# Performance work log

Measured on AMD Instinct MI355X. Metric: run time of the kernel, lower is better.

## Reference

```python
import jax, jax.numpy as jnp
import numpy as np


def setup_inputs() -> dict:
    key = jax.random.key(0)
    ks = jax.random.split(key, 5)
    b, f, h, w, c = 2, 16, 64, 64, 256
    heads, D = 8, 32
    hD = heads * D
    x = jax.random.normal(ks[0], (b, f, h, w, c), dtype=jnp.float32)
    s = 1.0 / np.sqrt(c)
    Wq = jax.random.normal(ks[1], (c, hD), dtype=jnp.float32) * s
    Wk = jax.random.normal(ks[2], (c, hD), dtype=jnp.float32) * s
    Wv = jax.random.normal(ks[3], (c, hD), dtype=jnp.float32) * s
    Wo = jax.random.normal(ks[4], (hD, c), dtype=jnp.float32) * s
    return {"x": x, "Wq": Wq, "Wk": Wk, "Wv": Wv, "Wo": Wo, "heads": heads}


def reference(x, Wq, Wk, Wv, Wo, heads):
    b, f, h, w, c = x.shape
    hD = Wq.shape[1]
    D = hD // heads
    n = h * w
    # fuse batch & frames; 1x1 conv == channel matmul
    xf = x.reshape(b * f, n, c)  # [(bf), n, c]

    def proj(W):
        # [(bf), n, hD] -> [(bf), heads, D, n]
        p = jnp.einsum('bnc,cd->bnd', xf, W)
        return p.reshape(b * f, n, heads, D).transpose(0, 2, 3, 1)

    q = jax.nn.softmax(proj(Wq), axis=-2)  # softmax over D (note: scale is dead code in source)
    k = jax.nn.softmax(proj(Wk), axis=-1)  # softmax over spatial n
    v = proj(Wv)
    context = jnp.einsum('bhdn,bhen->bhde', k, v)      # [(bf), heads, D, D]
    out = jnp.einsum('bhde,bhdn->bhen', context, q)    # [(bf), heads, D, n]
    out = out.transpose(0, 3, 1, 2).reshape(b * f, n, hD)
    out = jnp.einsum('bnd,dc->bnc', out, Wo)
    return out.reshape(b, f, h, w, c)
```

## Files before the change

kernel.cpp:

```cpp
#include <hip/hip_runtime.h>
#include <hip/hip_bf16.h>


typedef __attribute__((ext_vector_type(8))) short bf16x8;
typedef __attribute__((ext_vector_type(4))) float f32x4;

__device__ __forceinline__ unsigned short f2bf(float x) {
  __hip_bfloat16 h = __float2bfloat16(x);
  union { __hip_bfloat16 b; unsigned short u; } c; c.b = h; return c.u;
}

__global__ __launch_bounds__(256) void k0_prep(const float* __restrict__ Wq,
                                               const float* __restrict__ Wk,
                                               const float* __restrict__ Wv,
                                               unsigned short* __restrict__ WqT,
                                               unsigned short* __restrict__ WkvT) {
  int r = blockIdx.x, c = threadIdx.x;
  if (r < 256)      WqT [(r      )*256 + c] = f2bf(Wq[c*256 + r]);
  else if (r < 512) WkvT[(r - 256)*256 + c] = f2bf(Wk[c*256 + (r-256)]);
  else              WkvT[(r - 256)*256 + c] = f2bf(Wv[c*256 + (r-512)]);
}

__global__ __launch_bounds__(512, 2) void k1p(const float* __restrict__ x,
                                              const unsigned short* __restrict__ WkvT,
                                              float* __restrict__ ctxp) {
  __shared__ unsigned short As[2][32*256];
  __shared__ unsigned short slab[2][512*32];
  int bid = blockIdx.x;
  size_t rowbase = (size_t)bid * 256;
  int tid = threadIdx.x;
  int lane = tid & 63, wid = tid >> 6;
  int cl = lane & 15, rq = (lane >> 4) << 2, fs = lane >> 4;

  bf16x8 bfr[4][8];
#pragma unroll
  for (int nf = 0; nf < 4; ++nf)
#pragma unroll
    for (int kk = 0; kk < 8; ++kk)
      bfr[nf][kk] = *(const bf16x8*)(WkvT + (size_t)(wid*64 + nf*16 + cl)*256 + kk*32 + fs*8);

  f32x4 c2a = {}, c2b = {}, c2c = {}, c2d = {};
  f32x4 c3a = {}, c3b = {};
  bf16x8 bone;
#pragma unroll
  for (int j = 0; j < 8; ++j) bone[j] = (short)0x3F80;

  int ar = tid >> 5, as_ = tid & 31;
  int aw0 = ar*256 + ((as_ ^ (ar & 7)) << 3);
  int aw1 = (16 + ar)*256 + ((as_ ^ (ar & 7)) << 3);
  const float* ap = x + (rowbase + ar)*256 + as_*8;

  int ca0 = wid*32 + cl,        ca1 = wid*32 + 16 + cl;
  int cb0 = 256 + wid*32 + cl,  cb1 = 256 + wid*32 + 16 + cl;
  int ra0 = ca0*32 + ((fs ^ ((ca0 ^ (ca0 >> 2)) & 3)) << 3);
  int ra1 = ca1*32 + ((fs ^ ((ca1 ^ (ca1 >> 2)) & 3)) << 3);
  int rb0 = cb0*32 + ((fs ^ ((cb0 ^ (cb0 >> 2)) & 3)) << 3);
  int rb1 = cb1*32 + ((fs ^ ((cb1 ^ (cb1 >> 2)) & 3)) << 3);

  f32x4 acc0[4], acc1[4];

  float4 pa0 = *(const float4*)ap;
  float4 pa1 = *(const float4*)(ap + 4);
  float4 pa2 = *(const float4*)(ap + 16*256);
  float4 pa3 = *(const float4*)(ap + 16*256 + 4);
  {
    unsigned short* Ab = &As[0][0];
    union { ushort4 u4[2]; int4 i4; } pk;
    pk.u4[0].x = f2bf(pa0.x); pk.u4[0].y = f2bf(pa0.y); pk.u4[0].z = f2bf(pa0.z); pk.u4[0].w = f2bf(pa0.w);
    pk.u4[1].x = f2bf(pa1.x); pk.u4[1].y = f2bf(pa1.y); pk.u4[1].z = f2bf(pa1.z); pk.u4[1].w = f2bf(pa1.w);
    *(int4*)(&Ab[aw0]) = pk.i4;
    pk.u4[0].x = f2bf(pa2.x); pk.u4[0].y = f2bf(pa2.y); pk.u4[0].z = f2bf(pa2.z); pk.u4[0].w = f2bf(pa2.w);
    pk.u4[1].x = f2bf(pa3.x); pk.u4[1].y = f2bf(pa3.y); pk.u4[1].z = f2bf(pa3.z); pk.u4[1].w = f2bf(pa3.w);
    *(int4*)(&Ab[aw1]) = pk.i4;
  }
  {
    const float* apn = ap + 32*256;
    pa0 = *(const float4*)apn;
    pa1 = *(const float4*)(apn + 4);
    pa2 = *(const float4*)(apn + 16*256);
    pa3 = *(const float4*)(apn + 16*256 + 4);
  }
  __syncthreads();
  {
    unsigned short* Ab = &As[0][0];
#pragma unroll
    for (int ni = 0; ni < 4; ++ni) { acc0[ni] = (f32x4){}; acc1[ni] = (f32x4){}; }
#pragma unroll
    for (int kk = 0; kk < 8; ++kk) {
      int so = (((kk*4 + fs) ^ (cl & 7)) << 3);
      bf16x8 a0 = *(const bf16x8*)(&Ab[cl*256 + so]);
      bf16x8 a1 = *(const bf16x8*)(&Ab[(16 + cl)*256 + so]);
#pragma unroll
      for (int ni = 0; ni < 4; ++ni) {
        acc0[ni] = __builtin_amdgcn_mfma_f32_16x16x32_bf16(a0, bfr[ni][kk], acc0[ni], 0, 0, 0);
        acc1[ni] = __builtin_amdgcn_mfma_f32_16x16x32_bf16(a1, bfr[ni][kk], acc1[ni], 0, 0, 0);
      }
    }
  }

  for (int t = 0; t < 7; ++t) {
    {
      unsigned short* sb = &slab[t & 1][0];
#pragma unroll
      for (int ni = 0; ni < 4; ++ni) {
        int c = wid*64 + ni*16 + cl;
        int sw = (c ^ (c >> 2)) & 3;
        ushort4 w0, w1;
        if (wid < 4) {
          w0.x = f2bf(__expf(acc0[ni][0])); w0.y = f2bf(__expf(acc0[ni][1]));
          w0.z = f2bf(__expf(acc0[ni][2])); w0.w = f2bf(__expf(acc0[ni][3]));
          w1.x = f2bf(__expf(acc1[ni][0])); w1.y = f2bf(__expf(acc1[ni][1]));
          w1.z = f2bf(__expf(acc1[ni][2])); w1.w = f2bf(__expf(acc1[ni][3]));
        } else {
          w0.x = f2bf(acc0[ni][0]); w0.y = f2bf(acc0[ni][1]);
          w0.z = f2bf(acc0[ni][2]); w0.w = f2bf(acc0[ni][3]);
          w1.x = f2bf(acc1[ni][0]); w1.y = f2bf(acc1[ni][1]);
          w1.z = f2bf(acc1[ni][2]); w1.w = f2bf(acc1[ni][3]);
        }
        *(ushort4*)(&sb[c*32 + (((rq >> 3) ^ sw) << 3) + (rq & 7)]) = w0;
        *(ushort4*)(&sb[c*32 + ((((16 + rq) >> 3) ^ sw) << 3) + (rq & 7)]) = w1;
      }
    }
    {
      unsigned short* Ab = &As[(t + 1) & 1][0];
      union { ushort4 u4[2]; int4 i4; } pk;
      pk.u4[0].x = f2bf(pa0.x); pk.u4[0].y = f2bf(pa0.y); pk.u4[0].z = f2bf(pa0.z); pk.u4[0].w = f2bf(pa0.w);
      pk.u4[1].x = f2bf(pa1.x); pk.u4[1].y = f2bf(pa1.y); pk.u4[1].z = f2bf(pa1.z); pk.u4[1].w = f2bf(pa1.w);
      *(int4*)(&Ab[aw0]) = pk.i4;
      pk.u4[0].x = f2bf(pa2.x); pk.u4[0].y = f2bf(pa2.y); pk.u4[0].z = f2bf(pa2.z); pk.u4[0].w = f2bf(pa2.w);
      pk.u4[1].x = f2bf(pa3.x); pk.u4[1].y = f2bf(pa3.y); pk.u4[1].z = f2bf(pa3.z); pk.u4[1].w = f2bf(pa3.w);
      *(int4*)(&Ab[aw1]) = pk.i4;
    }
    if (t < 6) {
      const float* apn = ap + (size_t)(t + 2)*32*256;
      pa0 = *(const float4*)apn;
      pa1 = *(const float4*)(apn + 4);
      pa2 = *(const float4*)(apn + 16*256);
      pa3 = *(const float4*)(apn + 16*256 + 4);
    }
    __syncthreads();
    {
      unsigned short* sb = &slab[t & 1][0];
      bf16x8 af0 = *(const bf16x8*)(&sb[ra0]);
      bf16x8 af1 = *(const bf16x8*)(&sb[ra1]);
      bf16x8 bv0 = *(const bf16x8*)(&sb[rb0]);
      bf16x8 bv1 = *(const bf16x8*)(&sb[rb1]);
      c2a = __builtin_amdgcn_mfma_f32_16x16x32_bf16(af0, bv0, c2a, 0, 0, 0);
      c2b = __builtin_amdgcn_mfma_f32_16x16x32_bf16(af0, bv1, c2b, 0, 0, 0);
      c2c = __builtin_amdgcn_mfma_f32_16x16x32_bf16(af1, bv0, c2c, 0, 0, 0);
      c2d = __builtin_amdgcn_mfma_f32_16x16x32_bf16(af1, bv1, c2d, 0, 0, 0);
      c3a = __builtin_amdgcn_mfma_f32_16x16x32_bf16(af0, bone, c3a, 0, 0, 0);
      c3b = __builtin_amdgcn_mfma_f32_16x16x32_bf16(af1, bone, c3b, 0, 0, 0);
    }
    {
      unsigned short* Ab = &As[(t + 1) & 1][0];
#pragma unroll
      for (int ni = 0; ni < 4; ++ni) { acc0[ni] = (f32x4){}; acc1[ni] = (f32x4){}; }
#pragma unroll
      for (int kk = 0; kk < 8; ++kk) {
        int so = (((kk*4 + fs) ^ (cl & 7)) << 3);
        bf16x8 a0 = *(const bf16x8*)(&Ab[cl*256 + so]);
        bf16x8 a1 = *(const bf16x8*)(&Ab[(16 + cl)*256 + so]);
#pragma unroll
        for (int ni = 0; ni < 4; ++ni) {
          acc0[ni] = __builtin_amdgcn_mfma_f32_16x16x32_bf16(a0, bfr[ni][kk], acc0[ni], 0, 0, 0);
          acc1[ni] = __builtin_amdgcn_mfma_f32_16x16x32_bf16(a1, bfr[ni][kk], acc1[ni], 0, 0, 0);
        }
      }
    }
  }
  {
    unsigned short* sb = &slab[1][0];
#pragma unroll
    for (int ni = 0; ni < 4; ++ni) {
      int c = wid*64 + ni*16 + cl;
      int sw = (c ^ (c >> 2)) & 3;
      ushort4 w0, w1;
      if (wid < 4) {
        w0.x = f2bf(__expf(acc0[ni][0])); w0.y = f2bf(__expf(acc0[ni][1]));
        w0.z = f2bf(__expf(acc0[ni][2])); w0.w = f2bf(__expf(acc0[ni][3]));
        w1.x = f2bf(__expf(acc1[ni][0])); w1.y = f2bf(__expf(acc1[ni][1]));
        w1.z = f2bf(__expf(acc1[ni][2])); w1.w = f2bf(__expf(acc1[ni][3]));
      } else {
        w0.x = f2bf(acc0[ni][0]); w0.y = f2bf(acc0[ni][1]);
        w0.z = f2bf(acc0[ni][2]); w0.w = f2bf(acc0[ni][3]);
        w1.x = f2bf(acc1[ni][0]); w1.y = f2bf(acc1[ni][1]);
        w1.z = f2bf(acc1[ni][2]); w1.w = f2bf(acc1[ni][3]);
      }
      *(ushort4*)(&sb[c*32 + (((rq >> 3) ^ sw) << 3) + (rq & 7)]) = w0;
      *(ushort4*)(&sb[c*32 + ((((16 + rq) >> 3) ^ sw) << 3) + (rq & 7)]) = w1;
    }
  }
  __syncthreads();
  {
    unsigned short* sb = &slab[1][0];
    bf16x8 af0 = *(const bf16x8*)(&sb[ra0]);
    bf16x8 af1 = *(const bf16x8*)(&sb[ra1]);
    bf16x8 bv0 = *(const bf16x8*)(&sb[rb0]);
    bf16x8 bv1 = *(const bf16x8*)(&sb[rb1]);
    c2a = __builtin_amdgcn_mfma_f32_16x16x32_bf16(af0, bv0, c2a, 0, 0, 0);
    c2b = __builtin_amdgcn_mfma_f32_16x16x32_bf16(af0, bv1, c2b, 0, 0, 0);
    c2c = __builtin_amdgcn_mfma_f32_16x16x32_bf16(af1, bv0, c2c, 0, 0, 0);
    c2d = __builtin_amdgcn_mfma_f32_16x16x32_bf16(af1, bv1, c2d, 0, 0, 0);
    c3a = __builtin_amdgcn_mfma_f32_16x16x32_bf16(af0, bone, c3a, 0, 0, 0);
    c3b = __builtin_amdgcn_mfma_f32_16x16x32_bf16(af1, bone, c3b, 0, 0, 0);
  }
  float* cp = ctxp + ((size_t)bid*8 + wid)*1056;
#pragma unroll
  for (int r = 0; r < 4; ++r) {
    cp[(rq + r)*33 + cl]            = c2a[r];
    cp[(rq + r)*33 + 16 + cl]       = c2b[r];
    cp[(16 + rq + r)*33 + cl]       = c2c[r];
    cp[(16 + rq + r)*33 + 16 + cl]  = c2d[r];
  }
  if (cl == 0) {
#pragma unroll
    for (int r = 0; r < 4; ++r) {
      cp[(rq + r)*33 + 32]      = c3a[r];
      cp[(16 + rq + r)*33 + 32] = c3b[r];
    }
  }
}

__global__ __launch_bounds__(256) void k2b_w2(const float* __restrict__ ctxp,
                                              const float* __restrict__ Wo,
                                              unsigned short* __restrict__ W2t) {
  __shared__ float clds[32*33];
  int bid = blockIdx.x;
  int h = bid & 7, bfi = bid >> 3;
  int tid = threadIdx.x;
  for (int i = tid; i < 1056; i += 256) {
    float s = 0.f;
#pragma unroll
    for (int p = 0; p < 16; ++p)
      s += ctxp[((size_t)(bfi*16 + p)*8 + h)*1056 + i];
    clds[i] = s;
  }
  __syncthreads();
  float acc[32] = {};
#pragma unroll 4
  for (int e = 0; e < 32; ++e) {
    float w = Wo[(size_t)(h*32 + e)*256 + tid];
#pragma unroll
    for (int d = 0; d < 32; ++d) acc[d] += clds[d*33 + e] * w;
  }
  unsigned short* o = W2t + ((size_t)bfi*256 + tid)*256 + h*32;
#pragma unroll
  for (int d = 0; d < 32; ++d) o[d] = f2bf(acc[d] / clds[d*33 + 32]);
}

__global__ __launch_bounds__(512, 2) void k3s(const float* __restrict__ x,
                                              const unsigned short* __restrict__ WqT,
                                              const unsigned short* __restrict__ W2t,
                                              float* __restrict__ out) {
  __shared__ unsigned short As[2][32*256];
  __shared__ unsigned short Qs[2][32*256];
  int bid = blockIdx.x;
  size_t rowbase = (size_t)bid * 256;
  int bfi = bid >> 4;
  int tid = threadIdx.x;
  int lane = tid & 63, wid = tid >> 6;
  int cl = lane & 15, rq = (lane >> 4) << 2, fs = lane >> 4;

  bf16x8 bq[2][8], bw[2][8];
#pragma unroll
  for (int nf = 0; nf < 2; ++nf)
#pragma unroll
    for (int kk = 0; kk < 8; ++kk) {
      bq[nf][kk] = *(const bf16x8*)(WqT + (size_t)(wid*32 + nf*16 + cl)*256 + kk*32 + fs*8);
      bw[nf][kk] = *(const bf16x8*)(W2t + ((size_t)bfi*256 + wid*32 + nf*16 + cl)*256 + kk*32 + fs*8);
    }

  int ar = tid >> 5, as_ = tid & 31;
  int aw0 = ar*256 + ((as_ ^ (ar & 7)) << 3);
  int aw1 = (16 + ar)*256 + ((as_ ^ (ar & 7)) << 3);
  const float* ap = x + (rowbase + ar)*256 + as_*8;

  int qslotbase = wid*4 + (rq >> 3);
  ushort4 qpk[2][2];

  float4 pa0 = *(const float4*)ap;
  float4 pa1 = *(const float4*)(ap + 4);
  float4 pa2 = *(const float4*)(ap + 16*256);
  float4 pa3 = *(const float4*)(ap + 16*256 + 4);
  {
    unsigned short* Ab = &As[0][0];
    union { ushort4 u4[2]; int4 i4; } pk;
    pk.u4[0].x = f2bf(pa0.x); pk.u4[0].y = f2bf(pa0.y); pk.u4[0].z = f2bf(pa0.z); pk.u4[0].w = f2bf(pa0.w);
    pk.u4[1].x = f2bf(pa1.x); pk.u4[1].y = f2bf(pa1.y); pk.u4[1].z = f2bf(pa1.z); pk.u4[1].w = f2bf(pa1.w);
    *(int4*)(&Ab[aw0]) = pk.i4;
    pk.u4[0].x = f2bf(pa2.x); pk.u4[0].y = f2bf(pa2.y); pk.u4[0].z = f2bf(pa2.z); pk.u4[0].w = f2bf(pa2.w);
    pk.u4[1].x = f2bf(pa3.x); pk.u4[1].y = f2bf(pa3.y); pk.u4[1].z = f2bf(pa3.z); pk.u4[1].w = f2bf(pa3.w);
    *(int4*)(&Ab[aw1]) = pk.i4;
  }
  {
    const float* apn = ap + 32*256;
    pa0 = *(const float4*)apn;
    pa1 = *(const float4*)(apn + 4);
    pa2 = *(const float4*)(apn + 16*256);
    pa3 = *(const float4*)(apn + 16*256 + 4);
  }
  __syncthreads();
  {
    unsigned short* Ab = &As[0][0];
    f32x4 ql[2][2] = {};
#pragma unroll
    for (int kk = 0; kk < 8; ++kk) {
      int so = (((kk*4 + fs) ^ (cl & 7)) << 3);
      bf16x8 a0 = *(const bf16x8*)(&Ab[cl*256 + so]);
      bf16x8 a1 = *(const bf16x8*)(&Ab[(16 + cl)*256 + so]);
#pragma unroll
      for (int nf = 0; nf < 2; ++nf) {
        ql[0][nf] = __builtin_amdgcn_mfma_f32_16x16x32_bf16(bq[nf][kk], a0, ql[0][nf], 0, 0, 0);
        ql[1][nf] = __builtin_amdgcn_mfma_f32_16x16x32_bf16(bq[nf][kk], a1, ql[1][nf], 0, 0, 0);
      }
    }
#pragma unroll
    for (int m = 0; m < 2; ++m) {
      float e0[4], e1[4]; float s8 = 0.f;
#pragma unroll
      for (int r = 0; r < 4; ++r) { e0[r] = __expf(ql[m][0][r]); e1[r] = __expf(ql[m][1][r]); s8 += e0[r] + e1[r]; }
      float s = s8; s += __shfl_xor(s, 16); s += __shfl_xor(s, 32);
      float inv = 1.0f / s;
      qpk[m][0].x = f2bf(e0[0]*inv); qpk[m][0].y = f2bf(e0[1]*inv); qpk[m][0].z = f2bf(e0[2]*inv); qpk[m][0].w = f2bf(e0[3]*inv);
      qpk[m][1].x = f2bf(e1[0]*inv); qpk[m][1].y = f2bf(e1[1]*inv); qpk[m][1].z = f2bf(e1[2]*inv); qpk[m][1].w = f2bf(e1[3]*inv);
    }
  }
  for (int t = 0; t < 7; ++t) {
    {
      unsigned short* Ab = &As[(t + 1) & 1][0];
      union { ushort4 u4[2]; int4 i4; } pk;
      pk.u4[0].x = f2bf(pa0.x); pk.u4[0].y = f2bf(pa0.y); pk.u4[0].z = f2bf(pa0.z); pk.u4[0].w = f2bf(pa0.w);
      pk.u4[1].x = f2bf(pa1.x); pk.u4[1].y = f2bf(pa1.y); pk.u4[1].z = f2bf(pa1.z); pk.u4[1].w = f2bf(pa1.w);
      *(int4*)(&Ab[aw0]) = pk.i4;
      pk.u4[0].x = f2bf(pa2.x); pk.u4[0].y = f2bf(pa2.y); pk.u4[0].z = f2bf(pa2.z); pk.u4[0].w = f2bf(pa2.w);
      pk.u4[1].x = f2bf(pa3.x); pk.u4[1].y = f2bf(pa3.y); pk.u4[1].z = f2bf(pa3.z); pk.u4[1].w = f2bf(pa3.w);
      *(int4*)(&Ab[aw1]) = pk.i4;
    }
    {
      unsigned short* Qb = &Qs[t & 1][0];
#pragma unroll
      for (int m = 0; m < 2; ++m) {
        int row = m*16 + cl;
#pragma unroll
        for (int nf = 0; nf < 2; ++nf) {
          int slot = qslotbase + nf*2;
          *(ushort4*)(&Qb[row*256 + ((slot ^ (row & 7)) << 3) + (rq & 4)]) = qpk[m][nf];
        }
      }
    }
    if (t < 6) {
      const float* apn = ap + (size_t)(t + 2)*32*256;
      pa0 = *(const float4*)apn;
      pa1 = *(const float4*)(apn + 4);
      pa2 = *(const float4*)(apn + 16*256);
      pa3 = *(const float4*)(apn + 16*256 + 4);
    }
    __syncthreads();
    f32x4 oa[2][2] = {};
    {
      unsigned short* Qb = &Qs[t & 1][0];
#pragma unroll
      for (int kk = 0; kk < 8; ++kk) {
        int so = (((kk*4 + fs) ^ (cl & 7)) << 3);
        bf16x8 q0 = *(const bf16x8*)(&Qb[cl*256 + so]);
        bf16x8 q1 = *(const bf16x8*)(&Qb[(16 + cl)*256 + so]);
#pragma unroll
        for (int nf = 0; nf < 2; ++nf) {
          oa[0][nf] = __builtin_amdgcn_mfma_f32_16x16x32_bf16(bw[nf][kk], q0, oa[0][nf], 0, 0, 0);
          oa[1][nf] = __builtin_amdgcn_mfma_f32_16x16x32_bf16(bw[nf][kk], q1, oa[1][nf], 0, 0, 0);
        }
      }
    }
    {
      unsigned short* Ab = &As[(t + 1) & 1][0];
      f32x4 ql[2][2] = {};
#pragma unroll
      for (int kk = 0; kk < 8; ++kk) {
        int so = (((kk*4 + fs) ^ (cl & 7)) << 3);
        bf16x8 a0 = *(const bf16x8*)(&Ab[cl*256 + so]);
        bf16x8 a1 = *(const bf16x8*)(&Ab[(16 + cl)*256 + so]);
#pragma unroll
        for (int nf = 0; nf < 2; ++nf) {
          ql[0][nf] = __builtin_amdgcn_mfma_f32_16x16x32_bf16(bq[nf][kk], a0, ql[0][nf], 0, 0, 0);
          ql[1][nf] = __builtin_amdgcn_mfma_f32_16x16x32_bf16(bq[nf][kk], a1, ql[1][nf], 0, 0, 0);
        }
      }
#pragma unroll
      for (int m = 0; m < 2; ++m) {
        float e0[4], e1[4]; float s8 = 0.f;
#pragma unroll
        for (int r = 0; r < 4; ++r) { e0[r] = __expf(ql[m][0][r]); e1[r] = __expf(ql[m][1][r]); s8 += e0[r] + e1[r]; }
        float s = s8; s += __shfl_xor(s, 16); s += __shfl_xor(s, 32);
        float inv = 1.0f / s;
        qpk[m][0].x = f2bf(e0[0]*inv); qpk[m][0].y = f2bf(e0[1]*inv); qpk[m][0].z = f2bf(e0[2]*inv); qpk[m][0].w = f2bf(e0[3]*inv);
        qpk[m][1].x = f2bf(e1[0]*inv); qpk[m][1].y = f2bf(e1[1]*inv); qpk[m][1].z = f2bf(e1[2]*inv); qpk[m][1].w = f2bf(e1[3]*inv);
      }
    }
#pragma unroll
    for (int m = 0; m < 2; ++m)
#pragma unroll
      for (int nf = 0; nf < 2; ++nf)
        *(f32x4*)(&out[(rowbase + (size_t)t*32 + m*16 + cl)*256 + wid*32 + nf*16 + rq]) = oa[m][nf];
  }
  {
    unsigned short* Qb = &Qs[1][0];
#pragma unroll
    for (int m = 0; m < 2; ++m) {
      int row = m*16 + cl;
#pragma unroll
      for (int nf = 0; nf < 2; ++nf) {
        int slot = qslotbase + nf*2;
        *(ushort4*)(&Qb[row*256 + ((slot ^ (row & 7)) << 3) + (rq & 4)]) = qpk[m][nf];
      }
    }
  }
  __syncthreads();
  {
    unsigned short* Qb = &Qs[1][0];
    f32x4 oa[2][2] = {};
#pragma unroll
    for (int kk = 0; kk < 8; ++kk) {
      int so = (((kk*4 + fs) ^ (cl & 7)) << 3);
      bf16x8 q0 = *(const bf16x8*)(&Qb[cl*256 + so]);
      bf16x8 q1 = *(const bf16x8*)(&Qb[(16 + cl)*256 + so]);
#pragma unroll
      for (int nf = 0; nf < 2; ++nf) {
        oa[0][nf] = __builtin_amdgcn_mfma_f32_16x16x32_bf16(bw[nf][kk], q0, oa[0][nf], 0, 0, 0);
        oa[1][nf] = __builtin_amdgcn_mfma_f32_16x16x32_bf16(bw[nf][kk], q1, oa[1][nf], 0, 0, 0);
      }
    }
#pragma unroll
    for (int m = 0; m < 2; ++m)
#pragma unroll
      for (int nf = 0; nf < 2; ++nf)
        *(f32x4*)(&out[(rowbase + (size_t)7*32 + m*16 + cl)*256 + wid*32 + nf*16 + rq]) = oa[m][nf];
  }
}

extern "C" void kernel_launch(void* const* d_in, const int* in_sizes, int n_in,
                              void* d_out, int out_size, void* d_ws, size_t ws_size,
                              hipStream_t stream) {
  const float* x  = (const float*)d_in[0];
  const float* Wq = (const float*)d_in[1];
  const float* Wk = (const float*)d_in[2];
  const float* Wv = (const float*)d_in[3];
  const float* Wo = (const float*)d_in[4];
  float* out = (float*)d_out;

  unsigned short* WkvT = (unsigned short*)d_ws;
  unsigned short* WqT  = WkvT + 131072;
  unsigned short* W2t  = WqT  + 65536;
  float*          ctxp = (float*)(W2t + 2097152);

  k0_prep <<<768,  256, 0, stream>>>(Wq, Wk, Wv, WqT, WkvT);
  k1p     <<<512,  512, 0, stream>>>(x, WkvT, ctxp);
  k2b_w2  <<<256,  256, 0, stream>>>(ctxp, Wo, W2t);
  k3s     <<<512,  512, 0, stream>>>(x, WqT, W2t, out);
}
```

Baseline: 142.8 us.

## Widen k1 to 1024 threads, splitting K/V heads across more waves

The context kernel now runs 16 waves per block instead of 8. Each wave projects 32 K or V channels instead of 64, so per-wave register use for weight fragments and accumulators is halved and there are more waves to hide latency. The softmax denominator is now summed directly from the exponentials with lane shuffles, replacing the extra MFMA against a ones vector. In exchange the block uses 1024 threads with the same shared memory, which may limit how many blocks fit per CU, and each wave now writes only half of the per-head context tile.

```diff
diff --git a/kernel.cpp b/kernel.cpp
--- a/kernel.cpp
+++ b/kernel.cpp
@@ -21,79 +21,71 @@
   else              WkvT[(r - 256)*256 + c] = f2bf(Wv[c*256 + (r-512)]);
 }
 
-__global__ __launch_bounds__(512, 2) void k1p(const float* __restrict__ x,
-                                              const unsigned short* __restrict__ WkvT,
-                                              float* __restrict__ ctxp) {
+__global__ __launch_bounds__(1024, 4) void k1w(const float* __restrict__ x,
+                                               const unsigned short* __restrict__ WkvT,
+                                               float* __restrict__ ctxp) {
   __shared__ unsigned short As[2][32*256];
   __shared__ unsigned short slab[2][512*32];
   int bid = blockIdx.x;
   size_t rowbase = (size_t)bid * 256;
   int tid = threadIdx.x;
-  int lane = tid & 63, wid = tid >> 6;
+  int lane = tid & 63, w = tid >> 6;
   int cl = lane & 15, rq = (lane >> 4) << 2, fs = lane >> 4;
-
-  bf16x8 bfr[4][8];
-#pragma unroll
-  for (int nf = 0; nf < 4; ++nf)
+  int h = w & 7;
+  bool isV = w >= 8;
+
+  bf16x8 bfr[2][8];
+#pragma unroll
+  for (int ni = 0; ni < 2; ++ni)
 #pragma unroll
     for (int kk = 0; kk < 8; ++kk)
-      bfr[nf][kk] = *(const bf16x8*)(WkvT + (size_t)(wid*64 + nf*16 + cl)*256 + kk*32 + fs*8);
-
-  f32x4 c2a = {}, c2b = {}, c2c = {}, c2d = {};
-  f32x4 c3a = {}, c3b = {};
-  bf16x8 bone;
-#pragma unroll
-  for (int j = 0; j < 8; ++j) bone[j] = (short)0x3F80;
+      bfr[ni][kk] = *(const bf16x8*)(WkvT + (size_t)(w*32 + ni*16 + cl)*256 + kk*32 + fs*8);
+
+  f32x4 c2[2] = {};
+  float dena0 = 0.f, dena1 = 0.f;
 
   int ar = tid >> 5, as_ = tid & 31;
-  int aw0 = ar*256 + ((as_ ^ (ar & 7)) << 3);
-  int aw1 = (16 + ar)*256 + ((as_ ^ (ar & 7)) << 3);
+  int aw = ar*256 + ((as_ ^ (ar & 7)) << 3);
   const float* ap = x + (rowbase + ar)*256 + as_*8;
 
-  int ca0 = wid*32 + cl,        ca1 = wid*32 + 16 + cl;
-  int cb0 = 256 + wid*32 + cl,  cb1 = 256 + wid*32 + 16 + cl;
+  int ca0 = h*32 + cl, ca1 = h*32 + 16 + cl;
+  int cb  = 256 + h*32 + (isV ? 16 : 0) + cl;
   int ra0 = ca0*32 + ((fs ^ ((ca0 ^ (ca0 >> 2)) & 3)) << 3);
   int ra1 = ca1*32 + ((fs ^ ((ca1 ^ (ca1 >> 2)) & 3)) << 3);
-  int rb0 = cb0*32 + ((fs ^ ((cb0 ^ (cb0 >> 2)) & 3)) << 3);
-  int rb1 = cb1*32 + ((fs ^ ((cb1 ^ (cb1 >> 2)) & 3)) << 3);
-
-  f32x4 acc0[4], acc1[4];
+  int rb  = cb*32  + ((fs ^ ((cb  ^ (cb  >> 2)) & 3)) << 3);
+
+  f32x4 acc[2][2];
 
   float4 pa0 = *(const float4*)ap;
   float4 pa1 = *(const float4*)(ap + 4);
-  float4 pa2 = *(const float4*)(ap + 16*256);
-  float4 pa3 = *(const float4*)(ap + 16*256 + 4);
   {
     unsigned short* Ab = &As[0][0];
     union { ushort4 u4[2]; int4 i4; } pk;
     pk.u4[0].x = f2bf(pa0.x); pk.u4[0].y = f2bf(pa0.y); pk.u4[0].z = f2bf(pa0.z); pk.u4[0].w = f2bf(pa0.w);
     pk.u4[1].x = f2bf(pa1.x); pk.u4[1].y = f2bf(pa1.y); pk.u4[1].z = f2bf(pa1.z); pk.u4[1].w = f2bf(pa1.w);
-    *(int4*)(&Ab[aw0]) = pk.i4;
-    pk.u4[0].x = f2bf(pa2.x); pk.u4[0].y = f2bf(pa2.y); pk.u4[0].z = f2bf(pa2.z); pk.u4[0].w = f2bf(pa2.w);
-    pk.u4[1].x = f2bf(pa3.x); pk.u4[1].y = f2bf(pa3.y); pk.u4[1].z = f2bf(pa3.z); pk.u4[1].w = f2bf(pa3.w);
-    *(int4*)(&Ab[aw1]) = pk.i4;
+    *(int4*)(&Ab[aw]) = pk.i4;
   }
   {
     const float* apn = ap + 32*256;
     pa0 = *(const float4*)apn;
     pa1 = *(const float4*)(apn + 4);
-    pa2 = *(const float4*)(apn + 16*256);
-    pa3 = *(const float4*)(apn + 16*256 + 4);
   }
   __syncthreads();
   {
     unsigned short* Ab = &As[0][0];
 #pragma unroll
-    for (int ni = 0; ni < 4; ++ni) { acc0[ni] = (f32x4){}; acc1[ni] = (f32x4){}; }
+    for (int m = 0; m < 2; ++m)
+#pragma unroll
+      for (int ni = 0; ni < 2; ++ni) acc[m][ni] = (f32x4){};
 #pragma unroll
     for (int kk = 0; kk < 8; ++kk) {
       int so = (((kk*4 + fs) ^ (cl & 7)) << 3);
       bf16x8 a0 = *(const bf16x8*)(&Ab[cl*256 + so]);
       bf16x8 a1 = *(const bf16x8*)(&Ab[(16 + cl)*256 + so]);
 #pragma unroll
-      for (int ni = 0; ni < 4; ++ni) {
-        acc0[ni] = __builtin_amdgcn_mfma_f32_16x16x32_bf16(a0, bfr[ni][kk], acc0[ni], 0, 0, 0);
-        acc1[ni] = __builtin_amdgcn_mfma_f32_16x16x32_bf16(a1, bfr[ni][kk], acc1[ni], 0, 0, 0);
+      for (int ni = 0; ni < 2; ++ni) {
+        acc[0][ni] = __builtin_amdgcn_mfma_f32_16x16x32_bf16(a0, bfr[ni][kk], acc[0][ni], 0, 0, 0);
+        acc[1][ni] = __builtin_amdgcn_mfma_f32_16x16x32_bf16(a1, bfr[ni][kk], acc[1][ni], 0, 0, 0);
       }
     }
   }
@@ -102,23 +94,24 @@
     {
       unsigned short* sb = &slab[t & 1][0];
 #pragma unroll
-      for (int ni = 0; ni < 4; ++ni) {
-        int c = wid*64 + ni*16 + cl;
+      for (int ni = 0; ni < 2; ++ni) {
+        int c = w*32 + ni*16 + cl;
         int sw = (c ^ (c >> 2)) & 3;
-        ushort4 w0, w1;
-        if (wid < 4) {
-          w0.x = f2bf(__expf(acc0[ni][0])); w0.y = f2bf(__expf(acc0[ni][1]));
-          w0.z = f2bf(__expf(acc0[ni][2])); w0.w = f2bf(__expf(acc0[ni][3]));
-          w1.x = f2bf(__expf(acc1[ni][0])); w1.y = f2bf(__expf(acc1[ni][1]));
-          w1.z = f2bf(__expf(acc1[ni][2])); w1.w = f2bf(__expf(acc1[ni][3]));
-        } else {
-          w0.x = f2bf(acc0[ni][0]); w0.y = f2bf(acc0[ni][1]);
-          w0.z = f2bf(acc0[ni][2]); w0.w = f2bf(acc0[ni][3]);
-          w1.x = f2bf(acc1[ni][0]); w1.y = f2bf(acc1[ni][1]);
-          w1.z = f2bf(acc1[ni][2]); w1.w = f2bf(acc1[ni][3]);
-        }
-        *(ushort4*)(&sb[c*32 + (((rq >> 3) ^ sw) << 3) + (rq & 7)]) = w0;
-        *(ushort4*)(&sb[c*32 + ((((16 + rq) >> 3) ^ sw) << 3) + (rq & 7)]) = w1;
+#pragma unroll
+        for (int m = 0; m < 2; ++m) {
+          int n4 = m*16 + rq;
+          ushort4 wv;
+          if (!isV) {
+            float e0 = __expf(acc[m][ni][0]), e1 = __expf(acc[m][ni][1]);
+            float e2 = __expf(acc[m][ni][2]), e3 = __expf(acc[m][ni][3]);
+            if (ni == 0) dena0 += (e0 + e1) + (e2 + e3); else dena1 += (e0 + e1) + (e2 + e3);
+            wv.x = f2bf(e0); wv.y = f2bf(e1); wv.z = f2bf(e2); wv.w = f2bf(e3);
+          } else {
+            wv.x = f2bf(acc[m][ni][0]); wv.y = f2bf(acc[m][ni][1]);
+            wv.z = f2bf(acc[m][ni][2]); wv.w = f2bf(acc[m][ni][3]);
+          }
+          *(ushort4*)(&sb[c*32 + (((n4 >> 3) ^ sw) << 3) + (n4 & 7)]) = wv;
+        }
       }
     }
     {
@@ -126,45 +119,37 @@
       union { ushort4 u4[2]; int4 i4; } pk;
       pk.u4[0].x = f2bf(pa0.x); pk.u4[0].y = f2bf(pa0.y); pk.u4[0].z = f2bf(pa0.z); pk.u4[0].w = f2bf(pa0.w);
       pk.u4[1].x = f2bf(pa1.x); pk.u4[1].y = f2bf(pa1.y); pk.u4[1].z = f2bf(pa1.z); pk.u4[1].w = f2bf(pa1.w);
-      *(int4*)(&Ab[aw0]) = pk.i4;
-      pk.u4[0].x = f2bf(pa2.x); pk.u4[0].y = f2bf(pa2.y); pk.u4[0].z = f2bf(pa2.z); pk.u4[0].w = f2bf(pa2.w);
-      pk.u4[1].x = f2bf(pa3.x); pk.u4[1].y = f2bf(pa3.y); pk.u4[1].z = f2bf(pa3.z); pk.u4[1].w = f2bf(pa3.w);
-      *(int4*)(&Ab[aw1]) = pk.i4;
+      *(int4*)(&Ab[aw]) = pk.i4;
     }
     if (t < 6) {
       const float* apn = ap + (size_t)(t + 2)*32*256;
       pa0 = *(const float4*)apn;
       pa1 = *(const float4*)(apn + 4);
-      pa2 = *(const float4*)(apn + 16*256);
-      pa3 = *(const float4*)(apn + 16*256 + 4);
     }
     __syncthreads();
     {
       unsigned short* sb = &slab[t & 1][0];
       bf16x8 af0 = *(const bf16x8*)(&sb[ra0]);
       bf16x8 af1 = *(const bf16x8*)(&sb[ra1]);
-      bf16x8 bv0 = *(const bf16x8*)(&sb[rb0]);
-      bf16x8 bv1 = *(const bf16x8*)(&sb[rb1]);
-      c2a = __builtin_amdgcn_mfma_f32_16x16x32_bf16(af0, bv0, c2a, 0, 0, 0);
-      c2b = __builtin_amdgcn_mfma_f32_16x16x32_bf16(af0, bv1, c2b, 0, 0, 0);
-      c2c = __builtin_amdgcn_mfma_f32_16x16x32_bf16(af1, bv0, c2c, 0, 0, 0);
-      c2d = __builtin_amdgcn_mfma_f32_16x16x32_bf16(af1, bv1, c2d, 0, 0, 0);
-      c3a = __builtin_amdgcn_mfma_f32_16x16x32_bf16(af0, bone, c3a, 0, 0, 0);
-      c3b = __builtin_amdgcn_mfma_f32_16x16x32_bf16(af1, bone, c3b, 0, 0, 0);
+      bf16x8 bv  = *(const bf16x8*)(&sb[rb]);
+      c2[0] = __builtin_amdgcn_mfma_f32_16x16x32_bf16(af0, bv, c2[0], 0, 0, 0);
+      c2[1] = __builtin_amdgcn_mfma_f32_16x16x32_bf16(af1, bv, c2[1], 0, 0, 0);
     }
     {
       unsigned short* Ab = &As[(t + 1) & 1][0];
 #pragma unroll
-      for (int ni = 0; ni < 4; ++ni) { acc0[ni] = (f32x4){}; acc1[ni] = (f32x4){}; }
+      for (int m = 0; m < 2; ++m)
+#pragma unroll
+        for (int ni = 0; ni < 2; ++ni) acc[m][ni] = (f32x4){};
 #pragma unroll
       for (int kk = 0; kk < 8; ++kk) {
         int so = (((kk*4 + fs) ^ (cl & 7)) << 3);
         bf16x8 a0 = *(const bf16x8*)(&Ab[cl*256 + so]);
         bf16x8 a1 = *(const bf16x8*)(&Ab[(16 + cl)*256 + so]);
 #pragma unroll
-        for (int ni = 0; ni < 4; ++ni) {
-          acc0[ni] = __builtin_amdgcn_mfma_f32_16x16x32_bf16(a0, bfr[ni][kk], acc0[ni], 0, 0, 0);
-          acc1[ni] = __builtin_amdgcn_mfma_f32_16x16x32_bf16(a1, bfr[ni][kk], acc1[ni], 0, 0, 0);
+        for (int ni = 0; ni < 2; ++ni) {
+          acc[0][ni] = __builtin_amdgcn_mfma_f32_16x16x32_bf16(a0, bfr[ni][kk], acc[0][ni], 0, 0, 0);
+          acc[1][ni] = __builtin_amdgcn_mfma_f32_16x16x32_bf16(a1, bfr[ni][kk], acc[1][ni], 0, 0, 0);
         }
       }
     }
@@ -172,23 +157,24 @@
   {
     unsigned short* sb = &slab[1][0];
 #pragma unroll
-    for (int ni = 0; ni < 4; ++ni) {
-      int c = wid*64 + ni*16 + cl;
+    for (int ni = 0; ni < 2; ++ni) {
+      int c = w*32 + ni*16 + cl;
       int sw = (c ^ (c >> 2)) & 3;
-      ushort4 w0, w1;
-      if (wid < 4) {
-        w0.x = f2bf(__expf(acc0[ni][0])); w0.y = f2bf(__expf(acc0[ni][1]));
-        w0.z = f2bf(__expf(acc0[ni][2])); w0.w = f2bf(__expf(acc0[ni][3]));
-        w1.x = f2bf(__expf(acc1[ni][0])); w1.y = f2bf(__expf(acc1[ni][1]));
-        w1.z = f2bf(__expf(acc1[ni][2])); w1.w = f2bf(__expf(acc1[ni][3]));
-      } else {
-        w0.x = f2bf(acc0[ni][0]); w0.y = f2bf(acc0[ni][1]);
-        w0.z = f2bf(acc0[ni][2]); w0.w = f2bf(acc0[ni][3]);
-        w1.x = f2bf(acc1[ni][0]); w1.y = f2bf(acc1[ni][1]);
-        w1.z = f2bf(acc1[ni][2]); w1.w = f2bf(acc1[ni][3]);
-      }
-      *(ushort4*)(&sb[c*32 + (((rq >> 3) ^ sw) << 3) + (rq & 7)]) = w0;
-      *(ushort4*)(&sb[c*32 + ((((16 + rq) >> 3) ^ sw) << 3) + (rq & 7)]) = w1;
+#pragma unroll
+      for (int m = 0; m < 2; ++m) {
+        int n4 = m*16 + rq;
+        ushort4 wv;
+        if (!isV) {
+          float e0 = __expf(acc[m][ni][0]), e1 = __expf(acc[m][ni][1]);
+          float e2 = __expf(acc[m][ni][2]), e3 = __expf(acc[m][ni][3]);
+          if (ni == 0) dena0 += (e0 + e1) + (e2 + e3); else dena1 += (e0 + e1) + (e2 + e3);
+          wv.x = f2bf(e0); wv.y = f2bf(e1); wv.z = f2bf(e2); wv.w = f2bf(e3);
+        } else {
+          wv.x = f2bf(acc[m][ni][0]); wv.y = f2bf(acc[m][ni][1]);
+          wv.z = f2bf(acc[m][ni][2]); wv.w = f2bf(acc[m][ni][3]);
+        }
+        *(ushort4*)(&sb[c*32 + (((n4 >> 3) ^ sw) << 3) + (n4 & 7)]) = wv;
+      }
     }
   }
   __syncthreads();
@@ -196,28 +182,23 @@
     unsigned short* sb = &slab[1][0];
     bf16x8 af0 = *(const bf16x8*)(&sb[ra0]);
     bf16x8 af1 = *(const bf16x8*)(&sb[ra1]);
-    bf16x8 bv0 = *(const bf16x8*)(&sb[rb0]);
-    bf16x8 bv1 = *(const bf16x8*)(&sb[rb1]);
-    c2a = __builtin_amdgcn_mfma_f32_16x16x32_bf16(af0, bv0, c2a, 0, 0, 0);
-    c2b = __builtin_amdgcn_mfma_f32_16x16x32_bf16(af0, bv1, c2b, 0, 0, 0);
-    c2c = __builtin_amdgcn_mfma_f32_16x16x32_bf16(af1, bv0, c2c, 0, 0, 0);
-    c2d = __builtin_amdgcn_mfma_f32_16x16x32_bf16(af1, bv1, c2d, 0, 0, 0);
-    c3a = __builtin_amdgcn_mfma_f32_16x16x32_bf16(af0, bone, c3a, 0, 0, 0);
-    c3b = __builtin_amdgcn_mfma_f32_16x16x32_bf16(af1, bone, c3b, 0, 0, 0);
-  }
-  float* cp = ctxp + ((size_t)bid*8 + wid)*1056;
-#pragma unroll
-  for (int r = 0; r < 4; ++r) {
-    cp[(rq + r)*33 + cl]            = c2a[r];
-    cp[(rq + r)*33 + 16 + cl]       = c2b[r];
-    cp[(16 + rq + r)*33 + cl]       = c2c[r];
-    cp[(16 + rq + r)*33 + 16 + cl]  = c2d[r];
-  }
-  if (cl == 0) {
-#pragma unroll
-    for (int r = 0; r < 4; ++r) {
-      cp[(rq + r)*33 + 32]      = c3a[r];
-      cp[(16 + rq + r)*33 + 32] = c3b[r];
+    bf16x8 bv  = *(const bf16x8*)(&sb[rb]);
+    c2[0] = __builtin_amdgcn_mfma_f32_16x16x32_bf16(af0, bv, c2[0], 0, 0, 0);
+    c2[1] = __builtin_amdgcn_mfma_f32_16x16x32_bf16(af1, bv, c2[1], 0, 0, 0);
+  }
+  float* cp = ctxp + ((size_t)bid*8 + h)*1056;
+  int ec = isV ? 16 + cl : cl;
+#pragma unroll
+  for (int di = 0; di < 2; ++di)
+#pragma unroll
+    for (int r = 0; r < 4; ++r)
+      cp[(di*16 + rq + r)*33 + ec] = c2[di][r];
+  if (!isV) {
+    dena0 += __shfl_xor(dena0, 16); dena0 += __shfl_xor(dena0, 32);
+    dena1 += __shfl_xor(dena1, 16); dena1 += __shfl_xor(dena1, 32);
+    if (fs == 0) {
+      cp[cl*33 + 32]        = dena0;
+      cp[(16 + cl)*33 + 32] = dena1;
     }
   }
 }
@@ -453,8 +434,8 @@
   unsigned short* W2t  = WqT  + 65536;
   float*          ctxp = (float*)(W2t + 2097152);
 
-  k0_prep <<<768,  256, 0, stream>>>(Wq, Wk, Wv, WqT, WkvT);
-  k1p     <<<512,  512, 0, stream>>>(x, WkvT, ctxp);
-  k2b_w2  <<<256,  256, 0, stream>>>(ctxp, Wo, W2t);
-  k3s     <<<512,  512, 0, stream>>>(x, WqT, W2t, out);
-}
+  k0_prep <<<768,  256,  0, stream>>>(Wq, Wk, Wv, WqT, WkvT);
+  k1w     <<<512,  1024, 0, stream>>>(x, WkvT, ctxp);
+  k2b_w2  <<<256,  256,  0, stream>>>(ctxp, Wo, W2t);
+  k3s     <<<512,  512,  0, stream>>>(x, WqT, W2t, out);
+}
```

Result: no change. 141.1 us (-1.2%).
